# Kernel optimization log

Hardware: AMD Instinct MI355X
Metric: run time of the kernel (lower is better)

## Reference

```python
import jax, jax.numpy as jnp
import numpy as np

EMBED_DIM = 768
NUM_HEADS = 12
HEAD_DIM = EMBED_DIM // NUM_HEADS  # 64
B, N = 2, 3073
SCALE = HEAD_DIM ** -0.5


def setup_inputs() -> dict:
    key = jax.random.key(0)
    ks = jax.random.split(key, 6)
    s = EMBED_DIM ** -0.5
    return {
        "x": jax.random.normal(ks[0], (B, N, EMBED_DIM), dtype=jnp.float32),
        "qkv_w": jax.random.normal(ks[1], (3 * EMBED_DIM, EMBED_DIM), dtype=jnp.float32) * s,
        "proj_w": jax.random.normal(ks[2], (EMBED_DIM, EMBED_DIM), dtype=jnp.float32) * s,
        "proj_b": jax.random.normal(ks[3], (EMBED_DIM,), dtype=jnp.float32) * 0.02,
        "conv_w": jax.random.normal(ks[4], (HEAD_DIM, 1, 3, 3), dtype=jnp.float32) * 0.02,
        "conv_b": jax.random.normal(ks[5], (HEAD_DIM,), dtype=jnp.float32) * 0.02,
    }


def _local_pos_embed(v, conv_w, conv_b):
    # v: [B, H, N, C] with C = head_dim; drop cls token, fold to spatial grid
    b, h, n, c = v.shape
    u = int(((n - 1) // 12) ** 0.5)
    Hh, Ww = 4 * u, 3 * u
    xs = jnp.transpose(v[:, :, 1:], (0, 1, 3, 2)).reshape(b * h, c, Hh, Ww)
    pe = jax.lax.conv_general_dilated(
        xs, conv_w, window_strides=(1, 1), padding=((1, 1), (1, 1)),
        feature_group_count=c, dimension_numbers=("NCHW", "OIHW", "NCHW"))
    pe = pe + conv_b[None, :, None, None]
    pe = pe.reshape(b, h, c, n - 1).transpose(0, 1, 3, 2)  # [B,H,N-1,C]
    zeros = jnp.zeros((b, h, 1, c), dtype=pe.dtype)
    return jnp.concatenate([zeros, pe], axis=2)  # [B,H,N,C]


def reference(x, qkv_w, proj_w, proj_b, conv_w, conv_b):
    b, n, d = x.shape
    qkv = x @ qkv_w.T  # [B, N, 3D]
    qkv = qkv.reshape(b, n, 3, NUM_HEADS, HEAD_DIM).transpose(2, 0, 3, 1, 4)  # [3,B,H,N,Dh]
    q, k, v = qkv[0], qkv[1], qkv[2]
    scores = jnp.einsum("bhqd,bhkd->bhqk", q, k) * SCALE
    attn = jax.nn.softmax(scores, axis=-1)
    out = jnp.einsum("bham,bhmv->bhav", attn, v)  # [B,H,N,Dh]
    out = out + _local_pos_embed(v, conv_w, conv_b)
    out = out.transpose(0, 2, 1, 3).reshape(b, n, d)  # b h n d -> b n (h d)
    return out @ proj_w.T + proj_b
```

## Files before the change

kernel.cpp:

```cpp
#include <hip/hip_runtime.h>
#include <math.h>

#define NB 2
#define SEQ 3073
#define DIM 768
#define NH 12
#define DH 64
#define HHH 64
#define WWW 48
#define NPATCH 3072
#define QSCALE_L2E 0.18033688f
#define KSPLIT 1536

#define BHN (NB * NH)
#define MROWS (NB * SEQ)
#define MPAD 6272
#define CNT (BHN * SEQ * DH)
#define VTSTRIDE 3136

typedef __attribute__((ext_vector_type(8))) short s8v;
typedef __attribute__((ext_vector_type(4))) float f4v;
typedef __attribute__((ext_vector_type(4))) ushort u4v;

#define MFMA16(a, b, c) __builtin_amdgcn_mfma_f32_16x16x32_bf16((a), (b), (c), 0, 0, 0)

__device__ __forceinline__ ushort f2bf(float f) {
    unsigned x = __float_as_uint(f);
    return (ushort)((x + 0x7FFFu + ((x >> 16) & 1u)) >> 16);
}
__device__ __forceinline__ float bf2f(ushort u) {
    return __uint_as_float(((unsigned)u) << 16);
}

__device__ __forceinline__ s8v ldsFrag(const ushort* base, int row, int half, int t) {
    int byte = (row * 128 + half * 64 + t * 16) ^ ((row & 7) << 4);
    return *(const s8v*)((const char*)base + byte);
}

__global__ __launch_bounds__(256) void split_hilo(const float* __restrict__ in,
                                                  ushort* __restrict__ hi,
                                                  ushort* __restrict__ lo,
                                                  int n_in, int n_grp) {
    for (int g = blockIdx.x * 256 + threadIdx.x; g < n_grp; g += gridDim.x * 256) {
        int i0 = g * 4;
        float4 vv;
        if (i0 + 4 <= n_in) {
            vv = *(const float4*)(in + i0);
        } else {
            vv.x = (i0 + 0 < n_in) ? in[i0 + 0] : 0.f;
            vv.y = (i0 + 1 < n_in) ? in[i0 + 1] : 0.f;
            vv.z = (i0 + 2 < n_in) ? in[i0 + 2] : 0.f;
            vv.w = (i0 + 3 < n_in) ? in[i0 + 3] : 0.f;
        }
        float v[4] = {vv.x, vv.y, vv.z, vv.w};
        u4v hv, lv;
        #pragma unroll
        for (int j = 0; j < 4; ++j) {
            ushort hb = f2bf(v[j]);
            hv[j] = hb;
            lv[j] = f2bf(v[j] - bf2f(hb));
        }
        *(u4v*)(hi + i0) = hv;
        *(u4v*)(lo + i0) = lv;
    }
}

__device__ __forceinline__ void mfma_tile_768(const ushort* __restrict__ gAh,
                                              const ushort* __restrict__ gAl,
                                              const ushort* __restrict__ gBh,
                                              const ushort* __restrict__ gBl,
                                              ushort* Ah, ushort* Al,
                                              ushort* Bh, ushort* Bl,
                                              f4v acc[4][4]) {
    const int tid = threadIdx.x;
    const int lane = tid & 63;
    const int w = tid >> 6;
    const int lo = lane & 15, t = lane >> 4;
    const int wr = w >> 1, wc = w & 1;

    for (int k0 = 0; k0 < DIM; k0 += 64) {
        __syncthreads();
        #pragma unroll
        for (int i = 0; i < 4; ++i) {
            int s = tid + 256 * i;
            int r = s >> 3, c = s & 7;
            int byte = (r * 128 + c * 16) ^ ((r & 7) << 4);
            size_t go = (size_t)r * DIM + k0 + c * 8;
            s8v a0 = *(const s8v*)(gAh + go);
            s8v a1 = *(const s8v*)(gAl + go);
            s8v b0 = *(const s8v*)(gBh + go);
            s8v b1 = *(const s8v*)(gBl + go);
            *(s8v*)((char*)Ah + byte) = a0;
            *(s8v*)((char*)Al + byte) = a1;
            *(s8v*)((char*)Bh + byte) = b0;
            *(s8v*)((char*)Bl + byte) = b1;
        }
        __syncthreads();

        #pragma unroll
        for (int h = 0; h < 2; ++h) {
            s8v af_h[4], af_l[4];
            #pragma unroll
            for (int i = 0; i < 4; ++i) {
                int row = wr * 64 + i * 16 + lo;
                af_h[i] = ldsFrag(Ah, row, h, t);
                af_l[i] = ldsFrag(Al, row, h, t);
            }
            #pragma unroll
            for (int j = 0; j < 4; ++j) {
                int row = wc * 64 + j * 16 + lo;
                s8v bf_h = ldsFrag(Bh, row, h, t);
                s8v bf_l = ldsFrag(Bl, row, h, t);
                #pragma unroll
                for (int i = 0; i < 4; ++i) {
                    acc[i][j] = MFMA16(af_h[i], bf_h, acc[i][j]);
                    acc[i][j] = MFMA16(af_h[i], bf_l, acc[i][j]);
                    acc[i][j] = MFMA16(af_l[i], bf_h, acc[i][j]);
                }
            }
        }
    }
}

__device__ __forceinline__ void mfma_tile_768_a1(const ushort* __restrict__ gA,
                                                 const ushort* __restrict__ gBh,
                                                 const ushort* __restrict__ gBl,
                                                 ushort* Ah, ushort* Bh, ushort* Bl,
                                                 f4v acc[4][4]) {
    const int tid = threadIdx.x;
    const int lane = tid & 63;
    const int w = tid >> 6;
    const int lo = lane & 15, t = lane >> 4;
    const int wr = w >> 1, wc = w & 1;

    for (int k0 = 0; k0 < DIM; k0 += 64) {
        __syncthreads();
        #pragma unroll
        for (int i = 0; i < 4; ++i) {
            int s = tid + 256 * i;
            int r = s >> 3, c = s & 7;
            int byte = (r * 128 + c * 16) ^ ((r & 7) << 4);
            size_t go = (size_t)r * DIM + k0 + c * 8;
            s8v a0 = *(const s8v*)(gA + go);
            s8v b0 = *(const s8v*)(gBh + go);
            s8v b1 = *(const s8v*)(gBl + go);
            *(s8v*)((char*)Ah + byte) = a0;
            *(s8v*)((char*)Bh + byte) = b0;
            *(s8v*)((char*)Bl + byte) = b1;
        }
        __syncthreads();

        #pragma unroll
        for (int h = 0; h < 2; ++h) {
            s8v af[4];
            #pragma unroll
            for (int i = 0; i < 4; ++i)
                af[i] = ldsFrag(Ah, wr * 64 + i * 16 + lo, h, t);
            #pragma unroll
            for (int j = 0; j < 4; ++j) {
                int row = wc * 64 + j * 16 + lo;
                s8v bf_h = ldsFrag(Bh, row, h, t);
                s8v bf_l = ldsFrag(Bl, row, h, t);
                #pragma unroll
                for (int i = 0; i < 4; ++i) {
                    acc[i][j] = MFMA16(af[i], bf_h, acc[i][j]);
                    acc[i][j] = MFMA16(af[i], bf_l, acc[i][j]);
                }
            }
        }
    }
}

__global__ __launch_bounds__(256) void qkv_mfma(const ushort* __restrict__ xh,
                                                const ushort* __restrict__ wh,
                                                const ushort* __restrict__ wl,
                                                ushort* __restrict__ q_bf,
                                                ushort* __restrict__ k_bf,
                                                ushort* __restrict__ v_bf,
                                                ushort* __restrict__ vt) {
    __shared__ ushort Ah[8192], Bh[8192], Bl[8192];
    const int m0 = blockIdx.x * 128;
    const int nb = blockIdx.y;
    f4v acc[4][4] = {};
    mfma_tile_768_a1(xh + (size_t)m0 * DIM,
                     wh + (size_t)nb * 128 * DIM, wl + (size_t)nb * 128 * DIM,
                     Ah, Bh, Bl, acc);

    const int tid = threadIdx.x;
    const int lane = tid & 63;
    const int w = tid >> 6;
    const int lo = lane & 15, t = lane >> 4;
    const int wr = w >> 1, wc = w & 1;
    const int which = nb / 6;
    const int rr0 = (nb % 6) * 128;

    #pragma unroll
    for (int i = 0; i < 4; ++i) {
        #pragma unroll
        for (int r = 0; r < 4; ++r) {
            int m = m0 + wr * 64 + i * 16 + t * 4 + r;
            if (m >= MROWS) continue;
            int bb = m / SEQ;
            int row = m - bb * SEQ;
            #pragma unroll
            for (int j = 0; j < 4; ++j) {
                int rr = rr0 + wc * 64 + j * 16 + lo;
                int hh = rr >> 6, dd = rr & 63;
                size_t base = ((size_t)(bb * NH + hh) * SEQ + row) * DH + dd;
                float val = acc[i][j][r];
                if (which == 0) {
                    q_bf[base] = f2bf(val * QSCALE_L2E);
                } else if (which == 1) {
                    k_bf[base] = f2bf(val);
                } else {
                    ushort vb = f2bf(val);
                    v_bf[base] = vb;
                    vt[((size_t)(bb * NH + hh) * DH + dd) * VTSTRIDE + row] = vb;
                }
            }
        }
    }
}

__global__ __launch_bounds__(256) void proj_mfma(const ushort* __restrict__ ah,
                                                 const ushort* __restrict__ al,
                                                 const ushort* __restrict__ pwh,
                                                 const ushort* __restrict__ pwl,
                                                 const float* __restrict__ bias,
                                                 float* __restrict__ out) {
    __shared__ ushort Ah[8192], Al[8192], Bh[8192], Bl[8192];
    const int m0 = blockIdx.x * 128;
    const int nb = blockIdx.y;
    f4v acc[4][4] = {};
    mfma_tile_768(ah + (size_t)m0 * DIM, al + (size_t)m0 * DIM,
                  pwh + (size_t)nb * 128 * DIM, pwl + (size_t)nb * 128 * DIM,
                  Ah, Al, Bh, Bl, acc);

    const int tid = threadIdx.x;
    const int lane = tid & 63;
    const int w = tid >> 6;
    const int lo = lane & 15, t = lane >> 4;
    const int wr = w >> 1, wc = w & 1;

    #pragma unroll
    for (int i = 0; i < 4; ++i) {
        #pragma unroll
        for (int r = 0; r < 4; ++r) {
            int m = m0 + wr * 64 + i * 16 + t * 4 + r;
            if (m >= MROWS) continue;
            #pragma unroll
            for (int j = 0; j < 4; ++j) {
                int n = nb * 128 + wc * 64 + j * 16 + lo;
                out[(size_t)m * DIM + n] = acc[i][j][r] + bias[n];
            }
        }
    }
}

__global__ __launch_bounds__(128, 2) void attn_mfma(const ushort* __restrict__ qh,
                                                    const ushort* __restrict__ kh,
                                                    const ushort* __restrict__ vt,
                                                    float* __restrict__ o0,
                                                    float* __restrict__ o1,
                                                    float* __restrict__ pli) {
    __shared__ __align__(16) ushort Kh[4096];
    __shared__ __align__(16) ushort Vt[5120];
    __shared__ __align__(16) ushort Pl[2][2048];

    const int tid = threadIdx.x;
    const int w = tid >> 6;
    const int lane = tid & 63;
    const int lo = lane & 15;
    const int t = lane >> 4;
    const int bh = blockIdx.y;
    const int q0 = blockIdx.x * 64;
    const int z = blockIdx.z;
    const int kbeg = z * KSPLIT;
    const int kend = z ? SEQ : KSPLIT;

    {
        int rr = 64 + (tid >> 3);
        int col = (tid & 7) * 8;
        int byte = (rr * 128 + col * 2) ^ ((rr & 7) << 4);
        short v = (rr == 64) ? (short)0x3F80 : (short)0;
        s8v ones = {v, v, v, v, v, v, v, v};
        *(s8v*)((char*)Vt + byte) = ones;
    }

    s8v qf0[2], qf1[2];
    #pragma unroll
    for (int g = 0; g < 2; ++g) {
        int qr = q0 + w * 32 + g * 16 + lo;
        if (qr > SEQ - 1) qr = SEQ - 1;
        const size_t qoff = ((size_t)bh * SEQ + qr) * DH + t * 8;
        qf0[g] = *(const s8v*)(qh + qoff);
        qf1[g] = *(const s8v*)(qh + qoff + 32);
    }

    const int rr = tid >> 1;
    const int cc = (tid & 1) * 4;
    int sbyte[4];
    #pragma unroll
    for (int i = 0; i < 4; ++i)
        sbyte[i] = (rr * 128 + (cc + i) * 16) ^ ((rr & 7) << 4);
    const ushort* gk = kh + (size_t)bh * SEQ * DH;
    const ushort* gvb = vt + (size_t)bh * DH * VTSTRIDE;

    s8v pkh[4], pvv[4];
    #pragma unroll
    for (int i = 0; i < 4; ++i) {
        pkh[i] = *(const s8v*)(gk + (size_t)(kbeg + rr) * DH + (cc + i) * 8);
        pvv[i] = *(const s8v*)(gvb + (size_t)rr * VTSTRIDE + kbeg + (cc + i) * 8);
    }

    f4v o[2][5] = {};

    for (int k0 = kbeg; k0 < kend; k0 += 64) {
        #pragma unroll
        for (int i = 0; i < 4; ++i) {
            *(s8v*)((char*)Kh + sbyte[i]) = pkh[i];
            *(s8v*)((char*)Vt + sbyte[i]) = pvv[i];
        }
        __syncthreads();

        const int kn = k0 + 64;
        if (kn < SEQ) {
            #pragma unroll
            for (int i = 0; i < 4; ++i) {
                pkh[i] = *(const s8v*)(gk + (size_t)(kn + rr) * DH + (cc + i) * 8);
                pvv[i] = *(const s8v*)(gvb + (size_t)rr * VTSTRIDE + kn + (cc + i) * 8);
            }
        }

        f4v sv[2][4];
        __builtin_amdgcn_s_setprio(1);
        #pragma unroll
        for (int tc = 0; tc < 4; ++tc) {
            int row = tc * 16 + lo;
            s8v b0 = ldsFrag(Kh, row, 0, t);
            s8v b1 = ldsFrag(Kh, row, 1, t);
            #pragma unroll
            for (int g = 0; g < 2; ++g) {
                f4v a = {0.f, 0.f, 0.f, 0.f};
                a = MFMA16(b0, qf0[g], a);
                a = MFMA16(b1, qf1[g], a);
                sv[g][tc] = a;
            }
        }
        __builtin_amdgcn_s_setprio(0);

        if (k0 + 64 > SEQ) {
            #pragma unroll
            for (int tc = 0; tc < 4; ++tc)
                #pragma unroll
                for (int r = 0; r < 4; ++r)
                    if (k0 + tc * 16 + 4 * t + r >= SEQ) {
                        sv[0][tc][r] = -1e30f;
                        sv[1][tc][r] = -1e30f;
                    }
        }

        #pragma unroll
        for (int g = 0; g < 2; ++g) {
            int prow = g * 16 + lo;
            int rb = prow * 128 + t * 8;
            #pragma unroll
            for (int tc = 0; tc < 4; ++tc) {
                unsigned long long pk = 0;
                #pragma unroll
                for (int r = 0; r < 4; ++r) {
                    float p = exp2f(sv[g][tc][r]);
                    pk |= (unsigned long long)((__float_as_uint(p) + 0x8000u) >> 16)
                          << (16 * r);
                }
                int byte = (rb + tc * 32) ^ ((lo & 7) << 4);
                *(unsigned long long*)((char*)Pl[w] + byte) = pk;
            }
        }

        s8v pf0[2], pf1[2];
        #pragma unroll
        for (int g = 0; g < 2; ++g) {
            pf0[g] = ldsFrag(Pl[w], g * 16 + lo, 0, t);
            pf1[g] = ldsFrag(Pl[w], g * 16 + lo, 1, t);
        }
        __builtin_amdgcn_s_setprio(1);
        #pragma unroll
        for (int dt = 0; dt < 5; ++dt) {
            s8v v0 = ldsFrag(Vt, dt * 16 + lo, 0, t);
            s8v v1 = ldsFrag(Vt, dt * 16 + lo, 1, t);
            #pragma unroll
            for (int g = 0; g < 2; ++g) {
                o[g][dt] = MFMA16(pf0[g], v0, o[g][dt]);
                o[g][dt] = MFMA16(pf1[g], v1, o[g][dt]);
            }
        }
        __builtin_amdgcn_s_setprio(0);

        __syncthreads();
    }

    const int b = bh / NH;
    const int h = bh - b * NH;
    float* obase = z ? o1 : o0;
    float* lbase = pli + (size_t)z * BHN * SEQ;
    #pragma unroll
    for (int g = 0; g < 2; ++g) {
        #pragma unroll
        for (int r = 0; r < 4; ++r) {
            int row = q0 + w * 32 + g * 16 + t * 4 + r;
            if (row >= SEQ) continue;
            if (lo == 0)
                lbase[(size_t)bh * SEQ + row] = o[g][4][r];
            #pragma unroll
            for (int dt = 0; dt < 4; ++dt)
                obase[((size_t)(b * SEQ + row)) * DIM + h * DH + dt * 16 + lo] =
                    o[g][dt][r];
        }
    }
}

__global__ __launch_bounds__(256) void combine_att(const float* __restrict__ po1,
                                                   const float* __restrict__ pli,
                                                   float* __restrict__ att) {
    const int total = MROWS * DIM / 4;
    for (int i = blockIdx.x * 256 + threadIdx.x; i < total; i += gridDim.x * 256) {
        size_t e = (size_t)i * 4;
        int m = (int)(e / DIM);
        int d = (int)(e - (size_t)m * DIM);
        int b = m / SEQ;
        int row = m - b * SEQ;
        int h = d >> 6;
        size_t li = (size_t)(b * NH + h) * SEQ + row;
        float inv = 1.f / (pli[li] + pli[(size_t)BHN * SEQ + li]);
        float4 a = *(const float4*)(att + e);
        float4 p = *(const float4*)(po1 + e);
        float4 rs;
        rs.x = (a.x + p.x) * inv;
        rs.y = (a.y + p.y) * inv;
        rs.z = (a.z + p.z) * inv;
        rs.w = (a.w + p.w) * inv;
        *(float4*)(att + e) = rs;
    }
}

__global__ __launch_bounds__(256) void conv_pe(const ushort* __restrict__ v,
                                               const float* __restrict__ cw,
                                               const float* __restrict__ cb,
                                               float* __restrict__ att) {
    const int tid = threadIdx.x;
    const int c = tid & 63;
    const int tl = tid >> 6;
    const int blk = blockIdx.x;
    const int bh = blk / 768;
    const int pb = blk - bh * 768;
    const int p = pb * 4 + tl;
    const int y = p / WWW;
    const int x0 = p - y * WWW;

    const ushort* vb = v + (size_t)bh * SEQ * DH;
    float acc = cb[c];
    #pragma unroll
    for (int dy = -1; dy <= 1; ++dy) {
        int yy = y + dy;
        if (yy < 0 || yy >= HHH) continue;
        #pragma unroll
        for (int dx = -1; dx <= 1; ++dx) {
            int xx = x0 + dx;
            if (xx < 0 || xx >= WWW) continue;
            acc = fmaf(bf2f(vb[(size_t)(1 + yy * WWW + xx) * DH + c]),
                       cw[c * 9 + (dy + 1) * 3 + (dx + 1)], acc);
        }
    }
    const int b = bh / NH;
    const int h = bh - b * NH;
    att[((size_t)(b * SEQ + 1 + p)) * DIM + h * DH + c] += acc;
}

extern "C" void kernel_launch(void* const* d_in, const int* in_sizes, int n_in,
                              void* d_out, int out_size, void* d_ws, size_t ws_size,
                              hipStream_t stream) {
    const float* x      = (const float*)d_in[0];
    const float* qkv_w  = (const float*)d_in[1];
    const float* proj_w = (const float*)d_in[2];
    const float* proj_b = (const float*)d_in[3];
    const float* conv_w = (const float*)d_in[4];
    const float* conv_b = (const float*)d_in[5];
    float* out = (float*)d_out;

    ushort* ws = (ushort*)d_ws;
    size_t o = 0;
    ushort* xh  = ws + o; o += (size_t)MPAD * DIM;
    ushort* xl  = ws + o; o += (size_t)MPAD * DIM;
    ushort* wh  = ws + o; o += (size_t)2304 * DIM;
    ushort* wl  = ws + o; o += (size_t)2304 * DIM;
    ushort* pwh = ws + o; o += (size_t)DIM * DIM;
    ushort* pwl = ws + o; o += (size_t)DIM * DIM;
    ushort* q_bf = ws + o; o += CNT;
    ushort* k_bf = ws + o; o += CNT;
    ushort* v_bf = ws + o; o += CNT;
    ushort* vtb  = ws + o; o += (size_t)BHN * DH * VTSTRIDE;
    float*  att  = (float*)(ws + o);
    float* po1 = (float*)ws;
    float* pli = (float*)(ws + (size_t)MROWS * DIM * 2);

    split_hilo<<<2048, 256, 0, stream>>>(x, xh, xl, MROWS * DIM, MPAD * DIM / 4);
    split_hilo<<<1024, 256, 0, stream>>>(qkv_w, wh, wl, 2304 * DIM, 2304 * DIM / 4);
    split_hilo<<<512, 256, 0, stream>>>(proj_w, pwh, pwl, DIM * DIM, DIM * DIM / 4);

    qkv_mfma<<<dim3(49, 18), 256, 0, stream>>>(xh, wh, wl, q_bf, k_bf, v_bf, vtb);
    attn_mfma<<<dim3(49, BHN, 2), 128, 0, stream>>>(q_bf, k_bf, vtb, att, po1, pli);
    combine_att<<<2048, 256, 0, stream>>>(po1, pli, att);
    conv_pe<<<BHN * (NPATCH / 4), 256, 0, stream>>>(v_bf, conv_w, conv_b, att);

    split_hilo<<<2048, 256, 0, stream>>>(att, xh, xl, MROWS * DIM, MPAD * DIM / 4);
    proj_mfma<<<dim3(49, 6), 256, 0, stream>>>(xh, xl, pwh, pwl, proj_b, out);
}
```

Measured before the change: 296.4 us.

## Fuse conv/combine into bf16 activation, drop hi/lo split for proj input

The conv positional embedding now writes bf16 into a reused buffer. The split-K combine kernel adds it and writes a single bf16 activation directly, which removes the separate split_hilo pass over the attention output. The projection GEMM drops the low half of the A operand, going from 3 to 2 MFMAs per tile, and x is cast to bf16 only instead of split. The softmax packing uses the hardware v_cvt_pk_bf16_f32 instruction. All of this cuts memory traffic and MFMA work at the cost of lower activation precision.

```diff
diff --git a/kernel.cpp b/kernel.cpp
--- a/kernel.cpp
+++ b/kernel.cpp
@@ -31,16 +31,20 @@
 __device__ __forceinline__ float bf2f(ushort u) {
     return __uint_as_float(((unsigned)u) << 16);
 }
+__device__ __forceinline__ unsigned cvt_pk_bf16(float a, float b) {
+    unsigned r;
+    asm("v_cvt_pk_bf16_f32 %0, %1, %2" : "=v"(r) : "v"(a), "v"(b));
+    return r;
+}
 
 __device__ __forceinline__ s8v ldsFrag(const ushort* base, int row, int half, int t) {
     int byte = (row * 128 + half * 64 + t * 16) ^ ((row & 7) << 4);
     return *(const s8v*)((const char*)base + byte);
 }
 
-__global__ __launch_bounds__(256) void split_hilo(const float* __restrict__ in,
-                                                  ushort* __restrict__ hi,
-                                                  ushort* __restrict__ lo,
-                                                  int n_in, int n_grp) {
+__global__ __launch_bounds__(256) void cast_bf16(const float* __restrict__ in,
+                                                 ushort* __restrict__ out,
+                                                 int n_in, int n_grp) {
     for (int g = blockIdx.x * 256 + threadIdx.x; g < n_grp; g += gridDim.x * 256) {
         int i0 = g * 4;
         float4 vv;
@@ -52,6 +56,20 @@
             vv.z = (i0 + 2 < n_in) ? in[i0 + 2] : 0.f;
             vv.w = (i0 + 3 < n_in) ? in[i0 + 3] : 0.f;
         }
+        u4v hv;
+        hv[0] = f2bf(vv.x); hv[1] = f2bf(vv.y);
+        hv[2] = f2bf(vv.z); hv[3] = f2bf(vv.w);
+        *(u4v*)(out + i0) = hv;
+    }
+}
+
+__global__ __launch_bounds__(256) void split_hilo(const float* __restrict__ in,
+                                                  ushort* __restrict__ hi,
+                                                  ushort* __restrict__ lo,
+                                                  int n_in, int n_grp) {
+    for (int g = blockIdx.x * 256 + threadIdx.x; g < n_grp; g += gridDim.x * 256) {
+        int i0 = g * 4;
+        float4 vv = *(const float4*)(in + i0);
         float v[4] = {vv.x, vv.y, vv.z, vv.w};
         u4v hv, lv;
         #pragma unroll
@@ -62,63 +80,6 @@
         }
         *(u4v*)(hi + i0) = hv;
         *(u4v*)(lo + i0) = lv;
-    }
-}
-
-__device__ __forceinline__ void mfma_tile_768(const ushort* __restrict__ gAh,
-                                              const ushort* __restrict__ gAl,
-                                              const ushort* __restrict__ gBh,
-                                              const ushort* __restrict__ gBl,
-                                              ushort* Ah, ushort* Al,
-                                              ushort* Bh, ushort* Bl,
-                                              f4v acc[4][4]) {
-    const int tid = threadIdx.x;
-    const int lane = tid & 63;
-    const int w = tid >> 6;
-    const int lo = lane & 15, t = lane >> 4;
-    const int wr = w >> 1, wc = w & 1;
-
-    for (int k0 = 0; k0 < DIM; k0 += 64) {
-        __syncthreads();
-        #pragma unroll
-        for (int i = 0; i < 4; ++i) {
-            int s = tid + 256 * i;
-            int r = s >> 3, c = s & 7;
-            int byte = (r * 128 + c * 16) ^ ((r & 7) << 4);
-            size_t go = (size_t)r * DIM + k0 + c * 8;
-            s8v a0 = *(const s8v*)(gAh + go);
-            s8v a1 = *(const s8v*)(gAl + go);
-            s8v b0 = *(const s8v*)(gBh + go);
-            s8v b1 = *(const s8v*)(gBl + go);
-            *(s8v*)((char*)Ah + byte) = a0;
-            *(s8v*)((char*)Al + byte) = a1;
-            *(s8v*)((char*)Bh + byte) = b0;
-            *(s8v*)((char*)Bl + byte) = b1;
-        }
-        __syncthreads();
-
-        #pragma unroll
-        for (int h = 0; h < 2; ++h) {
-            s8v af_h[4], af_l[4];
-            #pragma unroll
-            for (int i = 0; i < 4; ++i) {
-                int row = wr * 64 + i * 16 + lo;
-                af_h[i] = ldsFrag(Ah, row, h, t);
-                af_l[i] = ldsFrag(Al, row, h, t);
-            }
-            #pragma unroll
-            for (int j = 0; j < 4; ++j) {
-                int row = wc * 64 + j * 16 + lo;
-                s8v bf_h = ldsFrag(Bh, row, h, t);
-                s8v bf_l = ldsFrag(Bl, row, h, t);
-                #pragma unroll
-                for (int i = 0; i < 4; ++i) {
-                    acc[i][j] = MFMA16(af_h[i], bf_h, acc[i][j]);
-                    acc[i][j] = MFMA16(af_h[i], bf_l, acc[i][j]);
-                    acc[i][j] = MFMA16(af_l[i], bf_h, acc[i][j]);
-                }
-            }
-        }
     }
 }
 
@@ -223,18 +184,17 @@
 }
 
 __global__ __launch_bounds__(256) void proj_mfma(const ushort* __restrict__ ah,
-                                                 const ushort* __restrict__ al,
                                                  const ushort* __restrict__ pwh,
                                                  const ushort* __restrict__ pwl,
                                                  const float* __restrict__ bias,
                                                  float* __restrict__ out) {
-    __shared__ ushort Ah[8192], Al[8192], Bh[8192], Bl[8192];
+    __shared__ ushort Ah[8192], Bh[8192], Bl[8192];
     const int m0 = blockIdx.x * 128;
     const int nb = blockIdx.y;
     f4v acc[4][4] = {};
-    mfma_tile_768(ah + (size_t)m0 * DIM, al + (size_t)m0 * DIM,
-                  pwh + (size_t)nb * 128 * DIM, pwl + (size_t)nb * 128 * DIM,
-                  Ah, Al, Bh, Bl, acc);
+    mfma_tile_768_a1(ah + (size_t)m0 * DIM,
+                     pwh + (size_t)nb * 128 * DIM, pwl + (size_t)nb * 128 * DIM,
+                     Ah, Bh, Bl, acc);
 
     const int tid = threadIdx.x;
     const int lane = tid & 63;
@@ -366,15 +326,15 @@
             int rb = prow * 128 + t * 8;
             #pragma unroll
             for (int tc = 0; tc < 4; ++tc) {
-                unsigned long long pk = 0;
-                #pragma unroll
-                for (int r = 0; r < 4; ++r) {
-                    float p = exp2f(sv[g][tc][r]);
-                    pk |= (unsigned long long)((__float_as_uint(p) + 0x8000u) >> 16)
-                          << (16 * r);
-                }
+                float p0 = exp2f(sv[g][tc][0]);
+                float p1 = exp2f(sv[g][tc][1]);
+                float p2 = exp2f(sv[g][tc][2]);
+                float p3 = exp2f(sv[g][tc][3]);
+                uint2 pk;
+                pk.x = cvt_pk_bf16(p0, p1);
+                pk.y = cvt_pk_bf16(p2, p3);
                 int byte = (rb + tc * 32) ^ ((lo & 7) << 4);
-                *(unsigned long long*)((char*)Pl[w] + byte) = pk;
+                *(uint2*)((char*)Pl[w] + byte) = pk;
             }
         }
 
@@ -420,9 +380,44 @@
     }
 }
 
-__global__ __launch_bounds__(256) void combine_att(const float* __restrict__ po1,
+__global__ __launch_bounds__(256) void conv_pe(const ushort* __restrict__ v,
+                                               const float* __restrict__ cw,
+                                               const float* __restrict__ cb,
+                                               ushort* __restrict__ pe) {
+    const int tid = threadIdx.x;
+    const int c = tid & 63;
+    const int tl = tid >> 6;
+    const int blk = blockIdx.x;
+    const int bh = blk / 768;
+    const int pb = blk - bh * 768;
+    const int p = pb * 4 + tl;
+    const int y = p / WWW;
+    const int x0 = p - y * WWW;
+
+    const ushort* vb = v + (size_t)bh * SEQ * DH;
+    float acc = cb[c];
+    #pragma unroll
+    for (int dy = -1; dy <= 1; ++dy) {
+        int yy = y + dy;
+        if (yy < 0 || yy >= HHH) continue;
+        #pragma unroll
+        for (int dx = -1; dx <= 1; ++dx) {
+            int xx = x0 + dx;
+            if (xx < 0 || xx >= WWW) continue;
+            acc = fmaf(bf2f(vb[(size_t)(1 + yy * WWW + xx) * DH + c]),
+                       cw[c * 9 + (dy + 1) * 3 + (dx + 1)], acc);
+        }
+    }
+    const int b = bh / NH;
+    const int h = bh - b * NH;
+    pe[((size_t)(b * SEQ + 1 + p)) * DIM + h * DH + c] = f2bf(acc);
+}
+
+__global__ __launch_bounds__(256) void combine_att(const float* __restrict__ o0,
+                                                   const float* __restrict__ o1,
                                                    const float* __restrict__ pli,
-                                                   float* __restrict__ att) {
+                                                   const ushort* __restrict__ pe,
+                                                   ushort* __restrict__ ah) {
     const int total = MROWS * DIM / 4;
     for (int i = blockIdx.x * 256 + threadIdx.x; i < total; i += gridDim.x * 256) {
         size_t e = (size_t)i * 4;
@@ -433,48 +428,21 @@
         int h = d >> 6;
         size_t li = (size_t)(b * NH + h) * SEQ + row;
         float inv = 1.f / (pli[li] + pli[(size_t)BHN * SEQ + li]);
-        float4 a = *(const float4*)(att + e);
-        float4 p = *(const float4*)(po1 + e);
-        float4 rs;
-        rs.x = (a.x + p.x) * inv;
-        rs.y = (a.y + p.y) * inv;
-        rs.z = (a.z + p.z) * inv;
-        rs.w = (a.w + p.w) * inv;
-        *(float4*)(att + e) = rs;
-    }
-}
-
-__global__ __launch_bounds__(256) void conv_pe(const ushort* __restrict__ v,
-                                               const float* __restrict__ cw,
-                                               const float* __restrict__ cb,
-                                               float* __restrict__ att) {
-    const int tid = threadIdx.x;
-    const int c = tid & 63;
-    const int tl = tid >> 6;
-    const int blk = blockIdx.x;
-    const int bh = blk / 768;
-    const int pb = blk - bh * 768;
-    const int p = pb * 4 + tl;
-    const int y = p / WWW;
-    const int x0 = p - y * WWW;
-
-    const ushort* vb = v + (size_t)bh * SEQ * DH;
-    float acc = cb[c];
-    #pragma unroll
-    for (int dy = -1; dy <= 1; ++dy) {
-        int yy = y + dy;
-        if (yy < 0 || yy >= HHH) continue;
-        #pragma unroll
-        for (int dx = -1; dx <= 1; ++dx) {
-            int xx = x0 + dx;
-            if (xx < 0 || xx >= WWW) continue;
-            acc = fmaf(bf2f(vb[(size_t)(1 + yy * WWW + xx) * DH + c]),
-                       cw[c * 9 + (dy + 1) * 3 + (dx + 1)], acc);
-        }
-    }
-    const int b = bh / NH;
-    const int h = bh - b * NH;
-    att[((size_t)(b * SEQ + 1 + p)) * DIM + h * DH + c] += acc;
+        float4 a = *(const float4*)(o0 + e);
+        float4 p = *(const float4*)(o1 + e);
+        float pv[4] = {0.f, 0.f, 0.f, 0.f};
+        if (row > 0) {
+            u4v pb = *(const u4v*)(pe + e);
+            #pragma unroll
+            for (int j = 0; j < 4; ++j) pv[j] = bf2f(pb[j]);
+        }
+        u4v rs;
+        rs[0] = f2bf(fmaf(a.x + p.x, inv, pv[0]));
+        rs[1] = f2bf(fmaf(a.y + p.y, inv, pv[1]));
+        rs[2] = f2bf(fmaf(a.z + p.z, inv, pv[2]));
+        rs[3] = f2bf(fmaf(a.w + p.w, inv, pv[3]));
+        *(u4v*)(ah + e) = rs;
+    }
 }
 
 extern "C" void kernel_launch(void* const* d_in, const int* in_sizes, int n_in,
@@ -491,7 +459,7 @@
     ushort* ws = (ushort*)d_ws;
     size_t o = 0;
     ushort* xh  = ws + o; o += (size_t)MPAD * DIM;
-    ushort* xl  = ws + o; o += (size_t)MPAD * DIM;
+    o += (size_t)MPAD * DIM;
     ushort* wh  = ws + o; o += (size_t)2304 * DIM;
     ushort* wl  = ws + o; o += (size_t)2304 * DIM;
     ushort* pwh = ws + o; o += (size_t)DIM * DIM;
@@ -500,19 +468,19 @@
     ushort* k_bf = ws + o; o += CNT;
     ushort* v_bf = ws + o; o += CNT;
     ushort* vtb  = ws + o; o += (size_t)BHN * DH * VTSTRIDE;
-    float*  att  = (float*)(ws + o);
-    float* po1 = (float*)ws;
-    float* pli = (float*)(ws + (size_t)MROWS * DIM * 2);
-
-    split_hilo<<<2048, 256, 0, stream>>>(x, xh, xl, MROWS * DIM, MPAD * DIM / 4);
+    float*  o0   = (float*)(ws + o);
+    float*  po1 = (float*)ws;
+    float*  pli = (float*)(ws + (size_t)MROWS * DIM * 2);
+    ushort* pe  = vtb;
+    ushort* ah  = q_bf;
+
+    cast_bf16<<<2048, 256, 0, stream>>>(x, xh, MROWS * DIM, MPAD * DIM / 4);
     split_hilo<<<1024, 256, 0, stream>>>(qkv_w, wh, wl, 2304 * DIM, 2304 * DIM / 4);
     split_hilo<<<512, 256, 0, stream>>>(proj_w, pwh, pwl, DIM * DIM, DIM * DIM / 4);
 
     qkv_mfma<<<dim3(49, 18), 256, 0, stream>>>(xh, wh, wl, q_bf, k_bf, v_bf, vtb);
-    attn_mfma<<<dim3(49, BHN, 2), 128, 0, stream>>>(q_bf, k_bf, vtb, att, po1, pli);
-    combine_att<<<2048, 256, 0, stream>>>(po1, pli, att);
-    conv_pe<<<BHN * (NPATCH / 4), 256, 0, stream>>>(v_bf, conv_w, conv_b, att);
-
-    split_hilo<<<2048, 256, 0, stream>>>(att, xh, xl, MROWS * DIM, MPAD * DIM / 4);
-    proj_mfma<<<dim3(49, 6), 256, 0, stream>>>(xh, xl, pwh, pwl, proj_b, out);
-}
+    attn_mfma<<<dim3(49, BHN, 2), 128, 0, stream>>>(q_bf, k_bf, vtb, o0, po1, pli);
+    conv_pe<<<BHN * (NPATCH / 4), 256, 0, stream>>>(v_bf, conv_w, conv_b, pe);
+    combine_att<<<2048, 256, 0, stream>>>(o0, po1, pli, pe, ah);
+    proj_mfma<<<dim3(49, 6), 256, 0, stream>>>(ah, pwh, pwl, proj_b, out);
+}
```

Result: faster. 269.9 us (-8.9%).
